# Performance work log

Hardware: AMD Instinct MI355X
Metric: run time of the kernel (lower is better)

Reference implementation:

```python
import jax, jax.numpy as jnp
import numpy as np
from jax import lax

# db6 filters (pywt convention). rec_lo are the standard Daubechies-12 scaling coefs.
REC_LO = np.array([0.11154074335008017, 0.4946238903983854, 0.7511339080215775,
                   0.3152503517092432, -0.22626469396516913, -0.12976686756709563,
                   0.09750160558707936, 0.02752286553001629, -0.031582039318031156,
                   0.0005538422009938016, 0.004777257511010651, -0.00107730108499558])
L = 12
# qmf: rec_hi[n] = (-1)^n * rec_lo[L-1-n]
REC_HI = np.array([(-1.0)**n * REC_LO[L - 1 - n] for n in range(L)])
DEC_LO = REC_LO[::-1].copy()
DEC_HI = REC_HI[::-1].copy()
J = 8  # level1
DN = ('NCH', 'OIH', 'NCH')

def _afb(x):
    # one analysis level, symmetric padding (matches pytorch_wavelets afb1d).
    B, C, N = x.shape
    outsize = (N + L - 1) // 2
    p = 2 * (outsize - 1) - N + L
    xp = jnp.pad(x, ((0, 0), (0, 0), (p // 2, p - p // 2)), mode='symmetric')
    # torch conv1d correlates with reversed dec filters == rec filters
    k = jnp.stack([jnp.asarray(REC_LO, x.dtype), jnp.asarray(REC_HI, x.dtype)])[:, None, :]
    y = lax.conv_general_dilated(xp.reshape(B * C, 1, -1), k, (2,), 'VALID',
                                 dimension_numbers=DN)  # (B*C, 2, outsize)
    y = y.reshape(B, C, 2, outsize)
    return y[:, :, 0], y[:, :, 1]

def _sfb(lo, hi):
    # one synthesis level: conv_transpose1d(stride=2, padding=L-2) with rec filters
    # == dilate-by-2, pad 1 each side, correlate with flipped rec (= dec) filters.
    B, C, N = lo.shape
    def up(z, k):
        kk = jnp.asarray(k, z.dtype)[None, None, :]
        return lax.conv_general_dilated(z.reshape(B * C, 1, N), kk, (1,), [(1, 1)],
                                        lhs_dilation=(2,), dimension_numbers=DN).reshape(B, C, -1)
    return up(lo, DEC_LO) + up(hi, DEC_HI)  # length 2N - L + 2

def setup_inputs() -> dict:
    key = jax.random.key(0)
    k1, k2, k3 = jax.random.split(key, 3)
    Cin, Cout = 64, 64
    scale = 1.0 / (Cin * Cout)
    x = jax.random.normal(k1, (256, Cin, 1024), dtype=jnp.float32)
    weights1 = scale * jax.random.uniform(k2, (Cin, Cout, J + 6), dtype=jnp.float32)
    weights2 = scale * jax.random.uniform(k3, (Cin, Cout, J + 6), dtype=jnp.float32)
    return {'x': x, 'weights1': weights1, 'weights2': weights2}

def reference(x, weights1, weights2):
    # DWT decompose: yh[0] finest ... yh[-1] coarsest (pytorch_wavelets order)
    lo = x
    highs = []
    for _ in range(J):
        lo, hi = _afb(lo)
        highs.append(hi)
    # channel mix on coarsest approx and coarsest detail
    lo = jnp.einsum('bix,iox->box', lo, weights1)
    highs[-1] = jnp.einsum('bix,iox->box', highs[-1], weights2)
    # IDWT reconstruct, trimming odd-length mismatches like pytorch_wavelets
    y = lo
    for hi in highs[::-1]:
        if y.shape[-1] > hi.shape[-1]:
            y = y[..., :hi.shape[-1]]
        y = _sfb(y, hi)
    return y
```

## Files before the change

### kernel.cpp

```cpp
#include <hip/hip_runtime.h>

typedef float f2 __attribute__((ext_vector_type(2)));
typedef _Float16 half_t;
typedef _Float16 h4 __attribute__((ext_vector_type(4)));
typedef _Float16 h8 __attribute__((ext_vector_type(8)));

static constexpr float REC_LO[12] = {
  0.11154074335008017f, 0.4946238903983854f, 0.7511339080215775f, 0.3152503517092432f,
  -0.22626469396516913f, -0.12976686756709563f, 0.09750160558707936f, 0.02752286553001629f,
  -0.031582039318031156f, 0.0005538422009938016f, 0.004777257511010651f, -0.00107730108499558f };
static constexpr float REC_HI[12] = {
  -0.00107730108499558f, -0.004777257511010651f, 0.0005538422009938016f, 0.031582039318031156f,
  0.02752286553001629f, -0.09750160558707936f, -0.12976686756709563f, 0.22626469396516913f,
  0.3152503517092432f, -0.7511339080215775f, 0.4946238903983854f, -0.11154074335008017f };
static constexpr float DEC_LO[12] = {
  -0.00107730108499558f, 0.004777257511010651f, 0.0005538422009938016f, -0.031582039318031156f,
  0.02752286553001629f, 0.09750160558707936f, -0.12976686756709563f, -0.22626469396516913f,
  0.3152503517092432f, 0.7511339080215775f, 0.4946238903983854f, 0.11154074335008017f };
static constexpr float DEC_HI[12] = {
  -0.11154074335008017f, 0.4946238903983854f, -0.7511339080215775f, 0.3152503517092432f,
  0.22626469396516913f, -0.12976686756709563f, -0.09750160558707936f, 0.02752286553001629f,
  0.031582039318031156f, 0.0005538422009938016f, -0.004777257511010651f, -0.00107730108499558f };

#define NROWS 16384
#define WPB 4


__global__ __launch_bounds__(256) void afb_fused(const float* __restrict__ x,
                                                 half_t* __restrict__ ws) {
  __shared__ float sA[WPB][548];
  __shared__ float sB[WPB][296];
  constexpr int LENS[9] = {1024, 517, 264, 137, 74, 42, 26, 18, 14};
  constexpr int HSTR[8] = {520, 264, 144, 80, 48, 32, 24, 16};
  constexpr int HOFF[8] = {0, 520, 784, 928, 1008, 1056, 1088, 1112};
  const int wid = threadIdx.x >> 6;
  const int lane = threadIdx.x & 63;
  const int row = blockIdx.x * WPB + wid;
  float* bufA = sA[wid];
  float* bufB = sB[wid];
  const float* xrow = x + (size_t)row * 1024;
  half_t* hi0 = ws + (size_t)row * 520;

  {
    const int q = lane;
    const int base = (q == 0) ? 0 : 16 * q - 12;
    float xv[28];
#pragma unroll
    for (int r = 0; r < 7; ++r) {
      float4 v = *reinterpret_cast<const float4*>(xrow + base + 4 * r);
      xv[4 * r] = v.x; xv[4 * r + 1] = v.y; xv[4 * r + 2] = v.z; xv[4 * r + 3] = v.w;
    }
    float w[26];
    if (q == 0) {
#pragma unroll
      for (int e = 0; e < 26; ++e) w[e] = xv[e < 10 ? 9 - e : e - 10];
    } else {
#pragma unroll
      for (int e = 0; e < 26; ++e) w[e] = xv[2 + e];
    }
    f2 a[8];
#pragma unroll
    for (int d = 0; d < 8; ++d) a[d] = (f2){0.f, 0.f};
#pragma unroll
    for (int k = 0; k < 12; ++k) {
      f2 c = (f2){REC_LO[k], REC_HI[k]};
#pragma unroll
      for (int d = 0; d < 8; ++d) a[d] += w[2 * d + k] * c;
    }
#pragma unroll
    for (int d = 0; d < 4; ++d)
      *reinterpret_cast<f2*>(bufA + 14 + 8 * q + 2 * d) = (f2){a[2 * d].x, a[2 * d + 1].x};
    h8 hh;
#pragma unroll
    for (int d = 0; d < 8; ++d) hh[d] = (half_t)a[d].y;
    *reinterpret_cast<h8*>(hi0 + 8 * q) = hh;
  }
  if (lane < 5) {
    const int i0 = 1014 + 2 * lane;
    float acL = 0.f, acH = 0.f;
#pragma unroll
    for (int k = 0; k < 12; ++k) {
      int idx = i0 + k;
      idx = min(idx, 2047 - idx);
      float v = xrow[idx];
      acL += v * REC_LO[k];
      acH += v * REC_HI[k];
    }
    bufA[14 + 512 + lane] = acL;
    hi0[512 + lane] = (half_t)acH;
  }
  if (lane < 21) {
    int d, s;
    if (lane < 10) { d = 13 - lane; s = 14 + lane; }
    else { int k = lane - 10; d = 14 + 517 + k; s = 14 + 516 - k; }
    bufA[d] = bufA[s];
  }

  if (lane < 33) {
    const float* pp = bufA + 16 * lane + 4;
    float xv[28];
#pragma unroll
    for (int r = 0; r < 7; ++r) {
      float4 v = *reinterpret_cast<const float4*>(pp + 4 * r);
      xv[4 * r] = v.x; xv[4 * r + 1] = v.y; xv[4 * r + 2] = v.z; xv[4 * r + 3] = v.w;
    }
    f2 a[8];
#pragma unroll
    for (int d = 0; d < 8; ++d) a[d] = (f2){0.f, 0.f};
#pragma unroll
    for (int k = 0; k < 12; ++k) {
      f2 c = (f2){REC_LO[k], REC_HI[k]};
#pragma unroll
      for (int d = 0; d < 8; ++d) a[d] += xv[2 * d + k] * c;
    }
#pragma unroll
    for (int d = 0; d < 4; ++d)
      *reinterpret_cast<f2*>(bufB + 14 + 8 * lane + 2 * d) = (f2){a[2 * d].x, a[2 * d + 1].x};
    h8 hh;
#pragma unroll
    for (int d = 0; d < 8; ++d) hh[d] = (half_t)a[d].y;
    *reinterpret_cast<h8*>(ws + (size_t)NROWS * 520 + (size_t)row * 264 + 8 * lane) = hh;
  }
  if (lane < 21) {
    int d, s;
    if (lane < 10) { d = 13 - lane; s = 14 + lane; }
    else { int k = lane - 10; d = 14 + 264 + k; s = 14 + 263 - k; }
    bufB[d] = bufB[s];
  }

  __syncthreads();

  const int gid = threadIdx.x >> 4;
  const int l16 = threadIdx.x & 15;
  const int sub2 = gid & 3;
  const int q2 = ((gid >> 2) << 4) + l16;
  const int prow = blockIdx.x * WPB + sub2;
  float* cur = sB[sub2];
  float* dst = sA[sub2];
#pragma unroll
  for (int j = 2; j < 8; ++j) {
    const int outN = LENS[j + 1];
    const int NCH = (outN + 3) / 4;
    half_t* hiRow = ws + (size_t)NROWS * HOFF[j] + (size_t)prow * HSTR[j];
    if (q2 < NCH) {
      const float* pp = cur + 8 * q2 + 4;
      float xv[20];
#pragma unroll
      for (int r = 0; r < 5; ++r) {
        float4 v = *reinterpret_cast<const float4*>(pp + 4 * r);
        xv[4 * r] = v.x; xv[4 * r + 1] = v.y; xv[4 * r + 2] = v.z; xv[4 * r + 3] = v.w;
      }
      f2 a0 = {0.f, 0.f}, a1 = {0.f, 0.f}, a2 = {0.f, 0.f}, a3 = {0.f, 0.f};
#pragma unroll
      for (int k = 0; k < 12; ++k) {
        f2 c = (f2){REC_LO[k], REC_HI[k]};
        a0 += xv[k] * c; a1 += xv[2 + k] * c; a2 += xv[4 + k] * c; a3 += xv[6 + k] * c;
      }
      if (j < 7) {
        *reinterpret_cast<f2*>(dst + 14 + 4 * q2) = (f2){a0.x, a1.x};
        *reinterpret_cast<f2*>(dst + 16 + 4 * q2) = (f2){a2.x, a3.x};
      } else {
        h4 hl; hl[0] = (half_t)a0.x; hl[1] = (half_t)a1.x; hl[2] = (half_t)a2.x; hl[3] = (half_t)a3.x;
        *reinterpret_cast<h4*>(ws + (size_t)NROWS * 1128 + (size_t)prow * 16 + 4 * q2) = hl;
      }
      h4 hh; hh[0] = (half_t)a0.y; hh[1] = (half_t)a1.y; hh[2] = (half_t)a2.y; hh[3] = (half_t)a3.y;
      *reinterpret_cast<h4*>(hiRow + 4 * q2) = hh;
    }
    if (j < 7) {
      if (j < 4) __syncthreads();
      if (gid < 4) {
        if (l16 < 10) dst[13 - l16] = dst[14 + l16];
        if (l16 < 11) dst[14 + outN + l16] = dst[14 + outN - 1 - l16];
      }
      if (j < 4) __syncthreads();
      float* t = cur; cur = dst; dst = t;
    }
  }
}

__global__ __launch_bounds__(256) void sfb_fused(const half_t* __restrict__ ws,
                                                 float* __restrict__ out) {
  __shared__ float sP[WPB][280];
  __shared__ float sQ[WPB][544];
  const int wid = threadIdx.x >> 6;
  const int lane = threadIdx.x & 63;

  {
    constexpr int LENSY[6] = {14, 18, 26, 42, 74, 137};
    constexpr int HSOFF[6] = {1144, 1088, 1056, 1008, 928, 784};
    constexpr int HSSTR[6] = {16, 24, 32, 48, 80, 144};
    const int gid = threadIdx.x >> 4;
    const int l16 = threadIdx.x & 15;
    const int sub = gid & 3;
    const int q1 = ((gid >> 2) << 4) + l16;
    const int prow = blockIdx.x * WPB + sub;
    float* cur = sP[sub];
    float* dst = sQ[sub];
    if (gid < 4 && l16 < 2) {
      h8 v = *reinterpret_cast<const h8*>(ws + (size_t)NROWS * 1160 + (size_t)prow * 16 + 8 * l16);
      *reinterpret_cast<float4*>(cur + 8 * l16) =
          make_float4((float)v[0], (float)v[1], (float)v[2], (float)v[3]);
      *reinterpret_cast<float4*>(cur + 8 * l16 + 4) =
          make_float4((float)v[4], (float)v[5], (float)v[6], (float)v[7]);
    }
#pragma unroll
    for (int s = 0; s < 6; ++s) {
      const int N = LENSY[s];
      const int NP = N - 5;
      const int PCH = (NP + 3) / 4;
      const half_t* hsrc = ws + (size_t)NROWS * HSOFF[s] + (size_t)prow * HSSTR[s];
      if (q1 < PCH) {
        const int m0 = 4 * q1;
        float lv[9];
        {
          float4 a = *reinterpret_cast<const float4*>(cur + m0);
          float4 b = *reinterpret_cast<const float4*>(cur + m0 + 4);
          lv[0] = a.x; lv[1] = a.y; lv[2] = a.z; lv[3] = a.w;
          lv[4] = b.x; lv[5] = b.y; lv[6] = b.z; lv[7] = b.w;
          lv[8] = cur[m0 + 8];
        }
        float hv[9];
        {
          h4 h0 = *reinterpret_cast<const h4*>(hsrc + m0);
          h4 h1 = *reinterpret_cast<const h4*>(hsrc + m0 + 4);
          half_t h2 = hsrc[m0 + 8];
          hv[0] = (float)h0[0]; hv[1] = (float)h0[1]; hv[2] = (float)h0[2]; hv[3] = (float)h0[3];
          hv[4] = (float)h1[0]; hv[5] = (float)h1[1]; hv[6] = (float)h1[2]; hv[7] = (float)h1[3];
          hv[8] = (float)h2;
        }
        f2 a0 = {0.f, 0.f}, a1 = {0.f, 0.f}, a2 = {0.f, 0.f}, a3 = {0.f, 0.f};
#pragma unroll
        for (int t = 0; t < 6; ++t) {
          f2 dl = (f2){DEC_LO[2 * t + 1], DEC_LO[2 * t]};
          f2 dh = (f2){DEC_HI[2 * t + 1], DEC_HI[2 * t]};
          a0 += lv[t] * dl + hv[t] * dh;
          a1 += lv[1 + t] * dl + hv[1 + t] * dh;
          a2 += lv[2 + t] * dl + hv[2 + t] * dh;
          a3 += lv[3 + t] * dl + hv[3 + t] * dh;
        }
        *reinterpret_cast<float4*>(dst + 2 * m0)     = make_float4(a0.x, a0.y, a1.x, a1.y);
        *reinterpret_cast<float4*>(dst + 2 * m0 + 4) = make_float4(a2.x, a2.y, a3.x, a3.y);
      }
      if (s == 3 || s == 4) __syncthreads();
      float* t = cur; cur = dst; dst = t;
    }
  }
  __syncthreads();

  const int row = blockIdx.x * WPB + wid;
  float* cur = sP[wid];
  float* dst = sQ[wid];
  {
    const half_t* hsrc = ws + (size_t)NROWS * 520 + (size_t)row * 264;
    const int m0 = 4 * lane;
    float lv[9];
    {
      float4 a = *reinterpret_cast<const float4*>(cur + m0);
      float4 b = *reinterpret_cast<const float4*>(cur + m0 + 4);
      lv[0] = a.x; lv[1] = a.y; lv[2] = a.z; lv[3] = a.w;
      lv[4] = b.x; lv[5] = b.y; lv[6] = b.z; lv[7] = b.w;
      lv[8] = cur[m0 + 8];
    }
    float hv[9];
    {
      h4 h0 = *reinterpret_cast<const h4*>(hsrc + m0);
      h4 h1 = *reinterpret_cast<const h4*>(hsrc + m0 + 4);
      half_t h2 = hsrc[m0 + 8];
      hv[0] = (float)h0[0]; hv[1] = (float)h0[1]; hv[2] = (float)h0[2]; hv[3] = (float)h0[3];
      hv[4] = (float)h1[0]; hv[5] = (float)h1[1]; hv[6] = (float)h1[2]; hv[7] = (float)h1[3];
      hv[8] = (float)h2;
    }
    f2 a0 = {0.f, 0.f}, a1 = {0.f, 0.f}, a2 = {0.f, 0.f}, a3 = {0.f, 0.f};
#pragma unroll
    for (int t = 0; t < 6; ++t) {
      f2 dl = (f2){DEC_LO[2 * t + 1], DEC_LO[2 * t]};
      f2 dh = (f2){DEC_HI[2 * t + 1], DEC_HI[2 * t]};
      a0 += lv[t] * dl + hv[t] * dh;
      a1 += lv[1 + t] * dl + hv[1 + t] * dh;
      a2 += lv[2 + t] * dl + hv[2 + t] * dh;
      a3 += lv[3 + t] * dl + hv[3 + t] * dh;
    }
    *reinterpret_cast<float4*>(dst + 2 * m0)     = make_float4(a0.x, a0.y, a1.x, a1.y);
    *reinterpret_cast<float4*>(dst + 2 * m0 + 4) = make_float4(a2.x, a2.y, a3.x, a3.y);
    if (lane < 3) {
      const int m = 256 + lane;
      float aE = 0.f, aO = 0.f;
#pragma unroll
      for (int t = 0; t < 6; ++t) {
        float lvv = cur[m + t];
        float hvv = (float)hsrc[m + t];
        aE += lvv * DEC_LO[2 * t + 1] + hvv * DEC_HI[2 * t + 1];
        aO += lvv * DEC_LO[2 * t]     + hvv * DEC_HI[2 * t];
      }
      *reinterpret_cast<f2*>(dst + 2 * m) = (f2){aE, aO};
    }
  }
  {
    const half_t* hsrc = ws + (size_t)row * 520;
    float* orow = out + (size_t)row * 1024;
#pragma unroll
    for (int q0 = 0; q0 < 128; q0 += 64) {
      const int m0 = 4 * (q0 + lane);
      float lv[9];
      {
        float4 a = *reinterpret_cast<const float4*>(dst + m0);
        float4 b = *reinterpret_cast<const float4*>(dst + m0 + 4);
        lv[0] = a.x; lv[1] = a.y; lv[2] = a.z; lv[3] = a.w;
        lv[4] = b.x; lv[5] = b.y; lv[6] = b.z; lv[7] = b.w;
        lv[8] = dst[m0 + 8];
      }
      float hv[9];
      {
        h4 h0 = *reinterpret_cast<const h4*>(hsrc + m0);
        h4 h1 = *reinterpret_cast<const h4*>(hsrc + m0 + 4);
        half_t h2 = hsrc[m0 + 8];
        hv[0] = (float)h0[0]; hv[1] = (float)h0[1]; hv[2] = (float)h0[2]; hv[3] = (float)h0[3];
        hv[4] = (float)h1[0]; hv[5] = (float)h1[1]; hv[6] = (float)h1[2]; hv[7] = (float)h1[3];
        hv[8] = (float)h2;
      }
      f2 a0 = {0.f, 0.f}, a1 = {0.f, 0.f}, a2 = {0.f, 0.f}, a3 = {0.f, 0.f};
#pragma unroll
      for (int t = 0; t < 6; ++t) {
        f2 dl = (f2){DEC_LO[2 * t + 1], DEC_LO[2 * t]};
        f2 dh = (f2){DEC_HI[2 * t + 1], DEC_HI[2 * t]};
        a0 += lv[t] * dl + hv[t] * dh;
        a1 += lv[1 + t] * dl + hv[1 + t] * dh;
        a2 += lv[2 + t] * dl + hv[2 + t] * dh;
        a3 += lv[3 + t] * dl + hv[3 + t] * dh;
      }
      *reinterpret_cast<float4*>(orow + 2 * m0)     = make_float4(a0.x, a0.y, a1.x, a1.y);
      *reinterpret_cast<float4*>(orow + 2 * m0 + 4) = make_float4(a2.x, a2.y, a3.x, a3.y);
    }
  }
}

__global__ void mix_both(half_t* __restrict__ ws, const float* __restrict__ w1,
                         const float* __restrict__ w2) {
  __shared__ float s_in[2][896];
  const int which = blockIdx.x >> 7;
  const half_t* in = ws + (size_t)NROWS * (which ? 1112 : 1128);
  const float* w = which ? w2 : w1;
  half_t* out = ws + (size_t)NROWS * (which ? 1144 : 1160);
  int b0 = (blockIdx.x & 127) * 2;
  int t = threadIdx.x;
  int i = t / 14, xx = t % 14;
#pragma unroll
  for (int bb = 0; bb < 2; ++bb)
    s_in[bb][t] = (float)in[((size_t)(b0 + bb) * 64 + i) * 16 + xx];
  __syncthreads();
  float acc0 = 0.f, acc1 = 0.f;
#pragma unroll 8
  for (int k = 0; k < 64; ++k) {
    float wv = w[k * 896 + t];
    acc0 += s_in[0][k * 14 + xx] * wv;
    acc1 += s_in[1][k * 14 + xx] * wv;
  }
  out[((size_t)b0 * 64 + i) * 16 + xx] = (half_t)acc0;
  out[((size_t)(b0 + 1) * 64 + i) * 16 + xx] = (half_t)acc1;
}

extern "C" void kernel_launch(void* const* d_in, const int* in_sizes, int n_in,
                              void* d_out, int out_size, void* d_ws, size_t ws_size,
                              hipStream_t stream) {
  (void)in_sizes; (void)n_in; (void)out_size; (void)ws_size;
  const float* x  = (const float*)d_in[0];
  const float* w1 = (const float*)d_in[1];
  const float* w2 = (const float*)d_in[2];
  float* out = (float*)d_out;
  half_t* ws = (half_t*)d_ws;

  afb_fused<<<NROWS / WPB, 64 * WPB, 0, stream>>>(x, ws);
  mix_both<<<256, 896, 0, stream>>>(ws, w1, w2);
  sfb_fused<<<NROWS / WPB, 64 * WPB, 0, stream>>>(ws, out);
}
```

Measured before the change: 59.74 us.

## Fuse channel-mix einsum into synthesis kernel, removing separate mix launch

Removes the standalone mix_both kernel. Each sfb_fused block now computes the coarsest-level channel mix for its four rows directly from the workspace and weights, with a two-way split reduction over input channels in shared memory, and feeds the results straight into the first synthesis stage. This drops one kernel launch and the fp16 round-trip of the mixed coefficients through global memory. In exchange, each block re-reads the coarse coefficients for its batch and a strided slice of the weights, and adds two extra block barriers before synthesis begins.

```diff
diff --git a/kernel.cpp b/kernel.cpp
--- a/kernel.cpp
+++ b/kernel.cpp
@@ -179,48 +179,78 @@
 }
 
 __global__ __launch_bounds__(256) void sfb_fused(const half_t* __restrict__ ws,
+                                                 const float* __restrict__ w1,
+                                                 const float* __restrict__ w2,
                                                  float* __restrict__ out) {
   __shared__ float sP[WPB][280];
   __shared__ float sQ[WPB][544];
+  __shared__ float pSum[2][4][14][2];
+  __shared__ float loM[4][18];
+  __shared__ float hmS[4][18];
   const int wid = threadIdx.x >> 6;
   const int lane = threadIdx.x & 63;
+  const int row0 = blockIdx.x * WPB;
+  const int t = threadIdx.x;
+
+  if (t < 224) {
+    const int h = t / 112;
+    const int r = t % 112;
+    const int kind = r / 56;
+    const int c = (r % 56) / 14;
+    const int xx = r % 14;
+    const int b = row0 >> 6;
+    const int cg = (row0 & 63) + c;
+    const half_t* inb = ws + (size_t)NROWS * (kind ? 1112 : 1128) +
+                        ((size_t)(b * 64 + 32 * h)) * 16 + xx;
+    const float* wb = (kind ? w2 : w1) + (size_t)(32 * h) * 896 + cg * 14 + xx;
+    float acc = 0.f;
+#pragma unroll 8
+    for (int i = 0; i < 32; ++i)
+      acc += (float)inb[(size_t)i * 16] * wb[(size_t)i * 896];
+    pSum[kind][c][xx][h] = acc;
+  }
+  __syncthreads();
+  if (t < 112) {
+    const int kind = t / 56;
+    const int c = (t % 56) / 14;
+    const int xx = t % 14;
+    float v = pSum[kind][c][xx][0] + pSum[kind][c][xx][1];
+    (kind ? hmS : loM)[c][xx] = v;
+  } else if (t < 144) {
+    const int u = t - 112;
+    (u & 16 ? hmS : loM)[(u >> 2) & 3][14 + (u & 3)] = 0.f;
+  }
+  __syncthreads();
 
   {
     constexpr int LENSY[6] = {14, 18, 26, 42, 74, 137};
-    constexpr int HSOFF[6] = {1144, 1088, 1056, 1008, 928, 784};
+    constexpr int HSOFF[6] = {0, 1088, 1056, 1008, 928, 784};
     constexpr int HSSTR[6] = {16, 24, 32, 48, 80, 144};
     const int gid = threadIdx.x >> 4;
     const int l16 = threadIdx.x & 15;
     const int sub = gid & 3;
     const int q1 = ((gid >> 2) << 4) + l16;
-    const int prow = blockIdx.x * WPB + sub;
+    const int prow = row0 + sub;
     float* cur = sP[sub];
     float* dst = sQ[sub];
-    if (gid < 4 && l16 < 2) {
-      h8 v = *reinterpret_cast<const h8*>(ws + (size_t)NROWS * 1160 + (size_t)prow * 16 + 8 * l16);
-      *reinterpret_cast<float4*>(cur + 8 * l16) =
-          make_float4((float)v[0], (float)v[1], (float)v[2], (float)v[3]);
-      *reinterpret_cast<float4*>(cur + 8 * l16 + 4) =
-          make_float4((float)v[4], (float)v[5], (float)v[6], (float)v[7]);
-    }
 #pragma unroll
     for (int s = 0; s < 6; ++s) {
       const int N = LENSY[s];
       const int NP = N - 5;
       const int PCH = (NP + 3) / 4;
-      const half_t* hsrc = ws + (size_t)NROWS * HSOFF[s] + (size_t)prow * HSSTR[s];
       if (q1 < PCH) {
         const int m0 = 4 * q1;
-        float lv[9];
-        {
+        float lv[9], hv[9];
+        if (s == 0) {
+#pragma unroll
+          for (int e = 0; e < 9; ++e) { lv[e] = loM[sub][m0 + e]; hv[e] = hmS[sub][m0 + e]; }
+        } else {
+          const half_t* hsrc = ws + (size_t)NROWS * HSOFF[s] + (size_t)prow * HSSTR[s];
           float4 a = *reinterpret_cast<const float4*>(cur + m0);
           float4 b = *reinterpret_cast<const float4*>(cur + m0 + 4);
           lv[0] = a.x; lv[1] = a.y; lv[2] = a.z; lv[3] = a.w;
           lv[4] = b.x; lv[5] = b.y; lv[6] = b.z; lv[7] = b.w;
           lv[8] = cur[m0 + 8];
-        }
-        float hv[9];
-        {
           h4 h0 = *reinterpret_cast<const h4*>(hsrc + m0);
           h4 h1 = *reinterpret_cast<const h4*>(hsrc + m0 + 4);
           half_t h2 = hsrc[m0 + 8];
@@ -230,24 +260,24 @@
         }
         f2 a0 = {0.f, 0.f}, a1 = {0.f, 0.f}, a2 = {0.f, 0.f}, a3 = {0.f, 0.f};
 #pragma unroll
-        for (int t = 0; t < 6; ++t) {
-          f2 dl = (f2){DEC_LO[2 * t + 1], DEC_LO[2 * t]};
-          f2 dh = (f2){DEC_HI[2 * t + 1], DEC_HI[2 * t]};
-          a0 += lv[t] * dl + hv[t] * dh;
-          a1 += lv[1 + t] * dl + hv[1 + t] * dh;
-          a2 += lv[2 + t] * dl + hv[2 + t] * dh;
-          a3 += lv[3 + t] * dl + hv[3 + t] * dh;
+        for (int tt = 0; tt < 6; ++tt) {
+          f2 dl = (f2){DEC_LO[2 * tt + 1], DEC_LO[2 * tt]};
+          f2 dh = (f2){DEC_HI[2 * tt + 1], DEC_HI[2 * tt]};
+          a0 += lv[tt] * dl + hv[tt] * dh;
+          a1 += lv[1 + tt] * dl + hv[1 + tt] * dh;
+          a2 += lv[2 + tt] * dl + hv[2 + tt] * dh;
+          a3 += lv[3 + tt] * dl + hv[3 + tt] * dh;
         }
         *reinterpret_cast<float4*>(dst + 2 * m0)     = make_float4(a0.x, a0.y, a1.x, a1.y);
         *reinterpret_cast<float4*>(dst + 2 * m0 + 4) = make_float4(a2.x, a2.y, a3.x, a3.y);
       }
       if (s == 3 || s == 4) __syncthreads();
-      float* t = cur; cur = dst; dst = t;
+      float* tp = cur; cur = dst; dst = tp;
     }
   }
   __syncthreads();
 
-  const int row = blockIdx.x * WPB + wid;
+  const int row = row0 + wid;
   float* cur = sP[wid];
   float* dst = sQ[wid];
   {
@@ -272,13 +302,13 @@
     }
     f2 a0 = {0.f, 0.f}, a1 = {0.f, 0.f}, a2 = {0.f, 0.f}, a3 = {0.f, 0.f};
 #pragma unroll
-    for (int t = 0; t < 6; ++t) {
-      f2 dl = (f2){DEC_LO[2 * t + 1], DEC_LO[2 * t]};
-      f2 dh = (f2){DEC_HI[2 * t + 1], DEC_HI[2 * t]};
-      a0 += lv[t] * dl + hv[t] * dh;
-      a1 += lv[1 + t] * dl + hv[1 + t] * dh;
-      a2 += lv[2 + t] * dl + hv[2 + t] * dh;
-      a3 += lv[3 + t] * dl + hv[3 + t] * dh;
+    for (int tt = 0; tt < 6; ++tt) {
+      f2 dl = (f2){DEC_LO[2 * tt + 1], DEC_LO[2 * tt]};
+      f2 dh = (f2){DEC_HI[2 * tt + 1], DEC_HI[2 * tt]};
+      a0 += lv[tt] * dl + hv[tt] * dh;
+      a1 += lv[1 + tt] * dl + hv[1 + tt] * dh;
+      a2 += lv[2 + tt] * dl + hv[2 + tt] * dh;
+      a3 += lv[3 + tt] * dl + hv[3 + tt] * dh;
     }
     *reinterpret_cast<float4*>(dst + 2 * m0)     = make_float4(a0.x, a0.y, a1.x, a1.y);
     *reinterpret_cast<float4*>(dst + 2 * m0 + 4) = make_float4(a2.x, a2.y, a3.x, a3.y);
@@ -286,11 +316,11 @@
       const int m = 256 + lane;
       float aE = 0.f, aO = 0.f;
 #pragma unroll
-      for (int t = 0; t < 6; ++t) {
-        float lvv = cur[m + t];
-        float hvv = (float)hsrc[m + t];
-        aE += lvv * DEC_LO[2 * t + 1] + hvv * DEC_HI[2 * t + 1];
-        aO += lvv * DEC_LO[2 * t]     + hvv * DEC_HI[2 * t];
+      for (int tt = 0; tt < 6; ++tt) {
+        float lvv = cur[m + tt];
+        float hvv = (float)hsrc[m + tt];
+        aE += lvv * DEC_LO[2 * tt + 1] + hvv * DEC_HI[2 * tt + 1];
+        aO += lvv * DEC_LO[2 * tt]     + hvv * DEC_HI[2 * tt];
       }
       *reinterpret_cast<f2*>(dst + 2 * m) = (f2){aE, aO};
     }
@@ -320,43 +350,18 @@
       }
       f2 a0 = {0.f, 0.f}, a1 = {0.f, 0.f}, a2 = {0.f, 0.f}, a3 = {0.f, 0.f};
 #pragma unroll
-      for (int t = 0; t < 6; ++t) {
-        f2 dl = (f2){DEC_LO[2 * t + 1], DEC_LO[2 * t]};
-        f2 dh = (f2){DEC_HI[2 * t + 1], DEC_HI[2 * t]};
-        a0 += lv[t] * dl + hv[t] * dh;
-        a1 += lv[1 + t] * dl + hv[1 + t] * dh;
-        a2 += lv[2 + t] * dl + hv[2 + t] * dh;
-        a3 += lv[3 + t] * dl + hv[3 + t] * dh;
+      for (int tt = 0; tt < 6; ++tt) {
+        f2 dl = (f2){DEC_LO[2 * tt + 1], DEC_LO[2 * tt]};
+        f2 dh = (f2){DEC_HI[2 * tt + 1], DEC_HI[2 * tt]};
+        a0 += lv[tt] * dl + hv[tt] * dh;
+        a1 += lv[1 + tt] * dl + hv[1 + tt] * dh;
+        a2 += lv[2 + tt] * dl + hv[2 + tt] * dh;
+        a3 += lv[3 + tt] * dl + hv[3 + tt] * dh;
       }
       *reinterpret_cast<float4*>(orow + 2 * m0)     = make_float4(a0.x, a0.y, a1.x, a1.y);
       *reinterpret_cast<float4*>(orow + 2 * m0 + 4) = make_float4(a2.x, a2.y, a3.x, a3.y);
     }
   }
-}
-
-__global__ void mix_both(half_t* __restrict__ ws, const float* __restrict__ w1,
-                         const float* __restrict__ w2) {
-  __shared__ float s_in[2][896];
-  const int which = blockIdx.x >> 7;
-  const half_t* in = ws + (size_t)NROWS * (which ? 1112 : 1128);
-  const float* w = which ? w2 : w1;
-  half_t* out = ws + (size_t)NROWS * (which ? 1144 : 1160);
-  int b0 = (blockIdx.x & 127) * 2;
-  int t = threadIdx.x;
-  int i = t / 14, xx = t % 14;
-#pragma unroll
-  for (int bb = 0; bb < 2; ++bb)
-    s_in[bb][t] = (float)in[((size_t)(b0 + bb) * 64 + i) * 16 + xx];
-  __syncthreads();
-  float acc0 = 0.f, acc1 = 0.f;
-#pragma unroll 8
-  for (int k = 0; k < 64; ++k) {
-    float wv = w[k * 896 + t];
-    acc0 += s_in[0][k * 14 + xx] * wv;
-    acc1 += s_in[1][k * 14 + xx] * wv;
-  }
-  out[((size_t)b0 * 64 + i) * 16 + xx] = (half_t)acc0;
-  out[((size_t)(b0 + 1) * 64 + i) * 16 + xx] = (half_t)acc1;
 }
 
 extern "C" void kernel_launch(void* const* d_in, const int* in_sizes, int n_in,
@@ -370,6 +375,5 @@
   half_t* ws = (half_t*)d_ws;
 
   afb_fused<<<NROWS / WPB, 64 * WPB, 0, stream>>>(x, ws);
-  mix_both<<<256, 896, 0, stream>>>(ws, w1, w2);
-  sfb_fused<<<NROWS / WPB, 64 * WPB, 0, stream>>>(ws, out);
+  sfb_fused<<<NROWS / WPB, 64 * WPB, 0, stream>>>(ws, w1, w2, out);
 }
```

Result: slower. 62.11 us (+4.0%).
